# Kernel optimization log

Measured on AMD Instinct MI355X. Metric: run time of the kernel, lower is better.

The kernel has to match this reference:

```python
import jax, jax.numpy as jnp
from jax import lax
import numpy as np

SEQ = 1024
VOCAB = 50000
EMB = 300
CAS_V, CAS_D = 8, 50
POS_V, POS_D = 48, 50
IN_DIM = EMB + CAS_D + POS_D  # 400
H = 512
T = 13  # num_classes / CRF tags


def setup_inputs() -> dict:
    key = jax.random.key(0)
    ks = jax.random.split(key, 16)
    s = lambda k, shape, sc=0.05: jax.random.normal(k, shape, dtype=jnp.float32) * sc
    return {
        "x": jax.random.randint(ks[0], (SEQ,), 0, VOCAB),
        "casing": jax.random.randint(ks[1], (SEQ,), 0, CAS_V),
        "pos": jax.random.randint(ks[2], (SEQ,), 0, POS_V),
        "h0": jnp.zeros((2, H), dtype=jnp.float32),
        "c0": jnp.zeros((2, H), dtype=jnp.float32),
        "W_emb": s(ks[3], (VOCAB, EMB)),
        "W_cas": s(ks[4], (CAS_V, CAS_D)),
        "W_pos": s(ks[5], (POS_V, POS_D)),
        "Wx_f": s(ks[6], (IN_DIM, 4 * H)),
        "Wh_f": s(ks[7], (H, 4 * H)),
        "b_f": jnp.zeros((4 * H,), dtype=jnp.float32),
        "Wx_b": s(ks[8], (IN_DIM, 4 * H)),
        "Wh_b": s(ks[9], (H, 4 * H)),
        "b_b": jnp.zeros((4 * H,), dtype=jnp.float32),
        "W_out": s(ks[10], (2 * H, T)),
        "b_out": jnp.zeros((T,), dtype=jnp.float32),
        "trans": s(ks[11], (T, T), 0.1),
        "start_trans": s(ks[12], (T,), 0.1),
        "end_trans": s(ks[13], (T,), 0.1),
    }


def _lstm_dir(feat, Wx, Wh, b, h0, c0, reverse):
    # feat: [L, IN_DIM]; precompute input projection for all steps
    pre = feat @ Wx + b  # [L, 4H]

    def step(carry, p):
        h, c = carry
        z = p + h @ Wh
        i, f, g, o = jnp.split(z, 4, axis=-1)
        c = jax.nn.sigmoid(f) * c + jax.nn.sigmoid(i) * jnp.tanh(g)
        h = jax.nn.sigmoid(o) * jnp.tanh(c)
        return (h, c), h

    _, hs = lax.scan(step, (h0, c0), pre, reverse=reverse)
    return hs  # [L, H]


def _viterbi(em, trans, start_trans, end_trans):
    # em: [L, T] emission (log) scores; max-plus DP
    score0 = start_trans + em[0]

    def fwd(score, e):
        total = score[:, None] + trans  # [T, T]: prev -> next
        best = jnp.max(total, axis=0) + e
        idx = jnp.argmax(total, axis=0)
        return best, idx

    final, hist = lax.scan(fwd, score0, em[1:])  # hist: [L-1, T]
    final = final + end_trans
    last = jnp.argmax(final)

    def back(tag, idx_row):
        return idx_row[tag], tag

    first, rest = lax.scan(back, last, hist, reverse=True)
    return jnp.concatenate([first[None], rest])  # [L] int


def reference(x, casing, pos, h0, c0, W_emb, W_cas, W_pos, Wx_f, Wh_f, b_f,
              Wx_b, Wh_b, b_b, W_out, b_out, trans, start_trans, end_trans):
    # AWD-LSTM encode (eval mode: dropout identity)
    feat = jnp.concatenate([W_emb[x], W_cas[casing], W_pos[pos]], axis=-1)  # [L, 400]
    hf = _lstm_dir(feat, Wx_f, Wh_f, b_f, h0[0], c0[0], reverse=False)
    hb = _lstm_dir(feat, Wx_b, Wh_b, b_b, h0[1], c0[1], reverse=True)
    o = jnp.concatenate([hf, hb], axis=-1) @ W_out + b_out  # [L, T]
    tag_scores = jax.nn.log_softmax(o, axis=1)
    path = _viterbi(tag_scores, trans, start_trans, end_trans)
    return tag_scores, path
```

## Files before the change

kernel.cpp:

```cpp
#include <hip/hip_runtime.h>
#include <hip/hip_bf16.h>
#include <math.h>

#define SEQ 1024
#define HID 512
#define FOURH 2048
#define IND 400
#define NT 13

#define NWG_DIR 32
#define LSTM_THREADS 512
#define JPW 16
#define WCOLS 64
#define TAG_INVALID 0xFFFFFFFFu

__device__ __forceinline__ float bf2f(unsigned short u) {
    union { unsigned u32; float f; } v;
    v.u32 = ((unsigned)u) << 16;
    return v.f;
}

__device__ __forceinline__ unsigned short f2bf(float f) {
    union { float f; unsigned u; } v;
    v.f = f;
    unsigned u = v.u;
    unsigned rounding = 0x7FFFu + ((u >> 16) & 1u);
    u += rounding;
    return (unsigned short)(u >> 16);
}

__device__ __forceinline__ float ldf(const void* p, size_t i, int isf32) {
    return isf32 ? ((const float*)p)[i] : bf2f(((const unsigned short*)p)[i]);
}

__device__ __forceinline__ float fsigm(float x) {
    return __builtin_amdgcn_rcpf(1.f + __builtin_amdgcn_exp2f(-1.44269504f * x));
}
__device__ __forceinline__ float ftanhf(float x) {
    return 1.f - 2.f * __builtin_amdgcn_rcpf(__builtin_amdgcn_exp2f(2.88539008f * x) + 1.f);
}
__device__ __forceinline__ float satz(float z) { return fminf(fmaxf(z, -60.f), 60.f); }

__global__ __launch_bounds__(64) void detect_kernel(const unsigned short* __restrict__ w,
                                                    int* __restrict__ flag,
                                                    unsigned* __restrict__ vcnt) {
    int lane = threadIdx.x;
    int cnt = 0;
    for (int i = 0; i < 4; ++i) {
        unsigned short u = w[2 * (lane * 4 + i)];
        int e = (u >> 7) & 0xFF;
        if (e >= 90 && e < 127) cnt++;
    }
#pragma unroll
    for (int off = 32; off >= 1; off >>= 1) cnt += __shfl_xor(cnt, off, 64);
    if (lane == 0) *flag = (cnt < 128) ? 1 : 0;
    if (lane == 1) *vcnt = 0;
}

__global__ __launch_bounds__(256) void pre_gemm_kernel(
        const int* __restrict__ x, const int* __restrict__ cas, const int* __restrict__ pos,
        const void* __restrict__ W_emb, const void* __restrict__ W_cas, const void* __restrict__ W_pos,
        const void* __restrict__ Wx_f, const void* __restrict__ b_f,
        const void* __restrict__ Wx_b, const void* __restrict__ b_b,
        unsigned short* __restrict__ pre, const int* __restrict__ dflag) {
    __shared__ float ftile[32 * IND];
    __shared__ int idxs[96];
    const int isf32 = *dflag;
    int dir = blockIdx.z;
    const void* Wx = dir ? Wx_b : Wx_f;
    const void* bb = dir ? b_b : b_f;
    unsigned short* pre_d = pre + (size_t)dir * SEQ * FOURH;
    int r0 = blockIdx.y * 32;
    int col = blockIdx.x * 256 + threadIdx.x;
    int tid = threadIdx.x;

    if (tid < 32)       idxs[tid] = x[r0 + tid];
    else if (tid < 64)  idxs[tid] = cas[r0 + tid - 32];
    else if (tid < 96)  idxs[tid] = pos[r0 + tid - 64];
    __syncthreads();

    for (int idx = tid; idx < 32 * IND; idx += 256) {
        int r = idx / IND;
        int e = idx - r * IND;
        float v;
        if (e < 300)      v = ldf(W_emb, (size_t)idxs[r] * 300 + e, isf32);
        else if (e < 350) v = ldf(W_cas, (size_t)idxs[32 + r] * 50 + (e - 300), isf32);
        else              v = ldf(W_pos, (size_t)idxs[64 + r] * 50 + (e - 350), isf32);
        ftile[idx] = v;
    }
    __syncthreads();

    float acc[32];
    float bias = ldf(bb, col, isf32);
#pragma unroll
    for (int r = 0; r < 32; ++r) acc[r] = bias;

    if (isf32) {
        const float* W = (const float*)Wx;
        for (int kk = 0; kk < 100; ++kk) {
            int k = kk * 4;
            float w0 = W[(size_t)(k + 0) * FOURH + col];
            float w1 = W[(size_t)(k + 1) * FOURH + col];
            float w2 = W[(size_t)(k + 2) * FOURH + col];
            float w3 = W[(size_t)(k + 3) * FOURH + col];
#pragma unroll
            for (int r = 0; r < 32; ++r) {
                float4 f = *(const float4*)&ftile[r * IND + k];
                acc[r] += f.x * w0 + f.y * w1 + f.z * w2 + f.w * w3;
            }
        }
    } else {
        const unsigned short* W = (const unsigned short*)Wx;
        for (int kk = 0; kk < 100; ++kk) {
            int k = kk * 4;
            float w0 = bf2f(W[(size_t)(k + 0) * FOURH + col]);
            float w1 = bf2f(W[(size_t)(k + 1) * FOURH + col]);
            float w2 = bf2f(W[(size_t)(k + 2) * FOURH + col]);
            float w3 = bf2f(W[(size_t)(k + 3) * FOURH + col]);
#pragma unroll
            for (int r = 0; r < 32; ++r) {
                float4 f = *(const float4*)&ftile[r * IND + k];
                acc[r] += f.x * w0 + f.y * w1 + f.z * w2 + f.w * w3;
            }
        }
    }
    for (int r = 0; r < 32; ++r) pre_d[(size_t)(r0 + r) * FOURH + col] = f2bf(acc[r]);
}

__global__ __launch_bounds__(LSTM_THREADS, 2) void lstm_kernel(
        const void* __restrict__ Wh_f, const void* __restrict__ Wh_b,
        const void* __restrict__ h0, const void* __restrict__ c0,
        const unsigned short* __restrict__ pre, float* __restrict__ hsout,
        unsigned long long* hbuf, const int* __restrict__ dflag) {
    __shared__ float red[2][8 * WCOLS];

    const int isf32 = *dflag;
    const int tid = threadIdx.x;
    const int b = blockIdx.x;
    const int dir = b & 1;
    const int g = b >> 1;
    const int j0 = g * JPW;

    const void* Wh = dir ? Wh_b : Wh_f;
    const unsigned short* pre_d = pre + (size_t)dir * SEQ * FOURH;
    float* hso = hsout + (size_t)dir * SEQ * HID;
    unsigned long long* hb_d = hbuf + dir * 2 * HID;

    const int seg  = tid >> 6;
    const int col  = tid & 63;
    const int unit = col & 15;
    const int gate = col >> 4;
    const int gcol = gate * HID + j0 + unit;
    const int redoff = seg * WCOLS + unit * 4 + gate;

    float4 w0, w1, w2, w3, w4, w5, w6, w7, w8, w9, w10, w11, w12, w13, w14, w15;
    if (isf32) {
        const float* wp = (const float*)Wh + (size_t)(seg * 64) * FOURH + gcol;
#define LDW(i) w##i = make_float4(wp[(size_t)(4*i+0)*FOURH], wp[(size_t)(4*i+1)*FOURH], \
                                  wp[(size_t)(4*i+2)*FOURH], wp[(size_t)(4*i+3)*FOURH])
        LDW(0); LDW(1); LDW(2); LDW(3); LDW(4); LDW(5); LDW(6); LDW(7);
        LDW(8); LDW(9); LDW(10); LDW(11); LDW(12); LDW(13); LDW(14); LDW(15);
#undef LDW
    } else {
        const unsigned short* wp = (const unsigned short*)Wh + (size_t)(seg * 64) * FOURH + gcol;
#define LDW(i) w##i = make_float4(bf2f(wp[(size_t)(4*i+0)*FOURH]), bf2f(wp[(size_t)(4*i+1)*FOURH]), \
                                  bf2f(wp[(size_t)(4*i+2)*FOURH]), bf2f(wp[(size_t)(4*i+3)*FOURH]))
        LDW(0); LDW(1); LDW(2); LDW(3); LDW(4); LDW(5); LDW(6); LDW(7);
        LDW(8); LDW(9); LDW(10); LDW(11); LDW(12); LDW(13); LDW(14); LDW(15);
#undef LDW
    }

    float creg = 0.f;
    unsigned short zn0 = 0, zn1 = 0, zn2 = 0, zn3 = 0;
    if (tid < JPW) {
        creg = ldf(c0, dir * HID + j0 + tid, isf32);
        float h0v = ldf(h0, dir * HID + j0 + tid, isf32);
        __hip_atomic_store(&hb_d[j0 + tid],
                           (unsigned long long)__float_as_uint(h0v),
                           __ATOMIC_RELAXED, __HIP_MEMORY_SCOPE_AGENT);
        __hip_atomic_store(&hb_d[HID + j0 + tid],
                           ((unsigned long long)TAG_INVALID << 32),
                           __ATOMIC_RELAXED, __HIP_MEMORY_SCOPE_AGENT);
        int t0 = dir ? (SEQ - 1) : 0;
        zn0 = pre_d[(size_t)t0 * FOURH + 0 * HID + j0 + tid];
        zn1 = pre_d[(size_t)t0 * FOURH + 1 * HID + j0 + tid];
        zn2 = pre_d[(size_t)t0 * FOURH + 2 * HID + j0 + tid];
        zn3 = pre_d[(size_t)t0 * FOURH + 3 * HID + j0 + tid];
    }
    __syncthreads();

    for (int s = 0; s < SEQ; ++s) {
        const int t = dir ? (SEQ - 1 - s) : s;

        unsigned hu;
        {
            const unsigned long long* wp = &hb_d[(s & 1) * HID + tid];
            const unsigned expect = (unsigned)s;
            unsigned long long w;
            do {
                w = __hip_atomic_load(wp, __ATOMIC_RELAXED, __HIP_MEMORY_SCOPE_AGENT);
            } while ((unsigned)(w >> 32) != expect);
            hu = (unsigned)w;
        }

        float zc0 = 0.f, zc1 = 0.f, zc2 = 0.f, zc3 = 0.f;
        if (tid < JPW) {
            zc0 = bf2f(zn0); zc1 = bf2f(zn1); zc2 = bf2f(zn2); zc3 = bf2f(zn3);
            if (s + 1 < SEQ) {
                int tn = dir ? (SEQ - 2 - s) : (s + 1);
                zn0 = pre_d[(size_t)tn * FOURH + 0 * HID + j0 + tid];
                zn1 = pre_d[(size_t)tn * FOURH + 1 * HID + j0 + tid];
                zn2 = pre_d[(size_t)tn * FOURH + 2 * HID + j0 + tid];
                zn3 = pre_d[(size_t)tn * FOURH + 3 * HID + j0 + tid];
            }
        }

        float a0 = 0.f, a1 = 0.f, a2 = 0.f, a3 = 0.f;
#define MACQ(i, A) { \
        float hx = __uint_as_float((unsigned)__builtin_amdgcn_readlane((int)hu, 4*i+0)); \
        float hy = __uint_as_float((unsigned)__builtin_amdgcn_readlane((int)hu, 4*i+1)); \
        float hz = __uint_as_float((unsigned)__builtin_amdgcn_readlane((int)hu, 4*i+2)); \
        float hw = __uint_as_float((unsigned)__builtin_amdgcn_readlane((int)hu, 4*i+3)); \
        A += hx * w##i.x + hy * w##i.y + hz * w##i.z + hw * w##i.w; }
        MACQ(0, a0)  MACQ(1, a1)  MACQ(2, a2)  MACQ(3, a3)
        MACQ(4, a0)  MACQ(5, a1)  MACQ(6, a2)  MACQ(7, a3)
        MACQ(8, a0)  MACQ(9, a1)  MACQ(10, a2) MACQ(11, a3)
        MACQ(12, a0) MACQ(13, a1) MACQ(14, a2) MACQ(15, a3)
#undef MACQ
        red[s & 1][redoff] = (a0 + a1) + (a2 + a3);
        __syncthreads();

        if (tid < JPW) {
            int jj = tid;
            float z0 = zc0, z1 = zc1, z2 = zc2, z3 = zc3;
            const float* rp = &red[s & 1][0];
#pragma unroll
            for (int s8 = 0; s8 < 8; ++s8) {
                float4 r4 = *(const float4*)&rp[s8 * WCOLS + jj * 4];
                z0 += r4.x; z1 += r4.y; z2 += r4.z; z3 += r4.w;
            }
            z0 = satz(z0); z1 = satz(z1); z2 = satz(z2); z3 = satz(z3);
            float ig = fsigm(z0);
            float fg = fsigm(z1);
            float gg = ftanhf(z2);
            float og = fsigm(z3);
            float cnew = fg * creg + ig * gg;
            creg = cnew;
            float hnew = og * ftanhf(satz(cnew));
            unsigned long long w = ((unsigned long long)(unsigned)(s + 1) << 32)
                                 | (unsigned long long)__float_as_uint(hnew);
            __hip_atomic_store(&hb_d[((s + 1) & 1) * HID + j0 + jj], w,
                               __ATOMIC_RELAXED, __HIP_MEMORY_SCOPE_AGENT);
            hso[(size_t)t * HID + j0 + jj] = hnew;
        }
    }
}

__global__ __launch_bounds__(64) void outproj_kernel(const float* __restrict__ hsout,
        const void* __restrict__ W_out, const void* __restrict__ b_out,
        float* __restrict__ out_scores,
        const void* __restrict__ trans, const void* __restrict__ strans,
        const void* __restrict__ etrans, float* __restrict__ out_path,
        unsigned* __restrict__ vcnt, const int* __restrict__ dflag) {
    __shared__ unsigned char hist[SEQ][NT];
    const int isf32 = *dflag;
    int t = blockIdx.x;
    int lane = threadIdx.x;
    const float* hf = hsout + (size_t)t * HID;
    const float* hb = hsout + (size_t)SEQ * HID + (size_t)t * HID;
    float acc[NT];
#pragma unroll
    for (int j = 0; j < NT; ++j) acc[j] = 0.f;
    for (int k = lane; k < HID; k += 64) {
        float a = hf[k], b2 = hb[k];
#pragma unroll
        for (int j = 0; j < NT; ++j)
            acc[j] += a * ldf(W_out, (size_t)k * NT + j, isf32)
                    + b2 * ldf(W_out, (size_t)(HID + k) * NT + j, isf32);
    }
#pragma unroll
    for (int off = 32; off >= 1; off >>= 1) {
#pragma unroll
        for (int j = 0; j < NT; ++j) acc[j] += __shfl_xor(acc[j], off, 64);
    }
    float o[NT];
    float m = -1e30f;
#pragma unroll
    for (int j = 0; j < NT; ++j) { o[j] = acc[j] + ldf(b_out, j, isf32); m = fmaxf(m, o[j]); }
    float lse = 0.f;
#pragma unroll
    for (int j = 0; j < NT; ++j) lse += expf(o[j] - m);
    lse = m + logf(lse);
    if (lane < NT)
        __hip_atomic_store(&out_scores[t * NT + lane], o[lane] - lse,
                           __ATOMIC_RELAXED, __HIP_MEMORY_SCOPE_AGENT);
    __builtin_amdgcn_s_waitcnt(0);

    unsigned old = 0;
    if (lane == 0) old = atomicAdd(vcnt, 1u);
    old = __shfl(old, 0, 64);
    if (old != SEQ - 1) return;

    const float* em = out_scores;
    int j = lane < NT ? lane : 0;
    float tr[NT];
#pragma unroll
    for (int i = 0; i < NT; ++i) tr[i] = ldf(trans, i * NT + j, isf32);
#define EML(tt) __hip_atomic_load(&em[(size_t)(tt) * NT + j], __ATOMIC_RELAXED, __HIP_MEMORY_SCOPE_AGENT)
    float score = ldf(strans, j, isf32) + EML(0);
    float c0 = EML(1), c1 = EML(2), c2 = EML(3), c3 = EML(4),
          c4 = EML(5), c5 = EML(6), c6 = EML(7), c7 = EML(8);
#define VSTEP(PE, TT) { \
    float best = -1e30f; int arg = 0; \
    _Pragma("unroll") \
    for (int i = 0; i < NT; ++i) { \
        float si = __shfl(score, i, 64); \
        float cand = si + tr[i]; \
        if (cand > best) { best = cand; arg = i; } \
    } \
    if (lane < NT) hist[TT][lane] = (unsigned char)arg; \
    score = best + PE; }
    for (int tb = 1; tb < SEQ; tb += 8) {
        int nb = tb + 8;
        float n0 = 0.f, n1 = 0.f, n2 = 0.f, n3 = 0.f, n4 = 0.f, n5 = 0.f, n6 = 0.f, n7 = 0.f;
        if (nb + 0 < SEQ) n0 = EML(nb + 0);
        if (nb + 1 < SEQ) n1 = EML(nb + 1);
        if (nb + 2 < SEQ) n2 = EML(nb + 2);
        if (nb + 3 < SEQ) n3 = EML(nb + 3);
        if (nb + 4 < SEQ) n4 = EML(nb + 4);
        if (nb + 5 < SEQ) n5 = EML(nb + 5);
        if (nb + 6 < SEQ) n6 = EML(nb + 6);
        if (nb + 7 < SEQ) n7 = EML(nb + 7);
        VSTEP(c0, tb + 0)
        if (tb + 1 < SEQ) VSTEP(c1, tb + 1)
        if (tb + 2 < SEQ) VSTEP(c2, tb + 2)
        if (tb + 3 < SEQ) VSTEP(c3, tb + 3)
        if (tb + 4 < SEQ) VSTEP(c4, tb + 4)
        if (tb + 5 < SEQ) VSTEP(c5, tb + 5)
        if (tb + 6 < SEQ) VSTEP(c6, tb + 6)
        if (tb + 7 < SEQ) VSTEP(c7, tb + 7)
        c0 = n0; c1 = n1; c2 = n2; c3 = n3; c4 = n4; c5 = n5; c6 = n6; c7 = n7;
    }
#undef VSTEP
#undef EML
    score += ldf(etrans, j, isf32);
    float bmax = -1e30f;
    int last = 0;
#pragma unroll
    for (int i = 0; i < NT; ++i) {
        float si = __shfl(score, i, 64);
        if (si > bmax) { bmax = si; last = i; }
    }
    if (lane == 0) {
        int cur = last;
        out_path[SEQ - 1] = (float)cur;
        for (int tt = SEQ - 1; tt >= 1; --tt) {
            cur = hist[tt][cur];
            out_path[tt - 1] = (float)cur;
        }
    }
}

extern "C" void kernel_launch(void* const* d_in, const int* in_sizes, int n_in,
                              void* d_out, int out_size, void* d_ws, size_t ws_size,
                              hipStream_t stream) {
    const int* x      = (const int*)d_in[0];
    const int* casing = (const int*)d_in[1];
    const int* posi   = (const int*)d_in[2];
    const void* h0    = d_in[3];
    const void* c0    = d_in[4];
    const void* W_emb = d_in[5];
    const void* W_cas = d_in[6];
    const void* W_pos = d_in[7];
    const void* Wx_f  = d_in[8];
    const void* Wh_f  = d_in[9];
    const void* b_f   = d_in[10];
    const void* Wx_b  = d_in[11];
    const void* Wh_b  = d_in[12];
    const void* b_b   = d_in[13];
    const void* W_out = d_in[14];
    const void* b_out = d_in[15];
    const void* trans = d_in[16];
    const void* strans = d_in[17];
    const void* etrans = d_in[18];

    char* ws = (char*)d_ws;
    int* dflag          = (int*)(ws + 448);
    unsigned* vcnt      = (unsigned*)(ws + 456);
    unsigned short* pre = (unsigned short*)(ws + 512);
    float* hsout        = (float*)(ws + 512 + 8388608);
    unsigned long long* hbuf = (unsigned long long*)(ws + 512 + 8388608 + 4194304);

    float* out_scores = (float*)d_out;
    float* out_path   = out_scores + SEQ * NT;

    detect_kernel<<<1, 64, 0, stream>>>((const unsigned short*)W_emb, dflag, vcnt);

    dim3 g2(8, 32, 2);
    pre_gemm_kernel<<<g2, 256, 0, stream>>>(x, casing, posi, W_emb, W_cas, W_pos,
                                            Wx_f, b_f, Wx_b, b_b, pre, dflag);

    lstm_kernel<<<2 * NWG_DIR, LSTM_THREADS, 0, stream>>>(
        Wh_f, Wh_b, h0, c0, pre, hsout, hbuf, dflag);

    outproj_kernel<<<SEQ, 64, 0, stream>>>(hsout, W_out, b_out, out_scores,
                                           trans, strans, etrans, out_path, vcnt, dflag);
}
```

Measured before the change: 2.334 ms.

## Replicate LSTM hidden-state exchange buffer per consumer workgroup to spread polling

The recurrent hidden-state handoff buffer is replicated once per workgroup in each direction. Each producer thread writes its new h value (tagged with the step number) into all 32 replicas, and each workgroup spin-polls only its own private copy. The goal is to stop all workgroups of a direction from polling the same cache lines, which should cut coherence traffic and latency in the per-step cross-workgroup sync. The first step now reads h0 directly instead of waiting on the buffer. The cost is 32 times more atomic stores per producer per step, and a much larger hbuf that the host allocation must supply.

```diff
diff --git a/kernel.cpp b/kernel.cpp
--- a/kernel.cpp
+++ b/kernel.cpp
@@ -144,7 +144,8 @@
     const void* Wh = dir ? Wh_b : Wh_f;
     const unsigned short* pre_d = pre + (size_t)dir * SEQ * FOURH;
     float* hso = hsout + (size_t)dir * SEQ * HID;
-    unsigned long long* hb_d = hbuf + dir * 2 * HID;
+    unsigned long long* hb_dir = hbuf + (size_t)dir * NWG_DIR * 2 * HID;
+    unsigned long long* hb_my  = hb_dir + (size_t)g * 2 * HID;
 
     const int seg  = tid >> 6;
     const int col  = tid & 63;
@@ -170,17 +171,19 @@
 #undef LDW
     }
 
+    const unsigned hu0 = __float_as_uint(ldf(h0, dir * HID + tid, isf32));
+
     float creg = 0.f;
     unsigned short zn0 = 0, zn1 = 0, zn2 = 0, zn3 = 0;
     if (tid < JPW) {
         creg = ldf(c0, dir * HID + j0 + tid, isf32);
-        float h0v = ldf(h0, dir * HID + j0 + tid, isf32);
-        __hip_atomic_store(&hb_d[j0 + tid],
-                           (unsigned long long)__float_as_uint(h0v),
-                           __ATOMIC_RELAXED, __HIP_MEMORY_SCOPE_AGENT);
-        __hip_atomic_store(&hb_d[HID + j0 + tid],
-                           ((unsigned long long)TAG_INVALID << 32),
-                           __ATOMIC_RELAXED, __HIP_MEMORY_SCOPE_AGENT);
+        const unsigned long long iv = ((unsigned long long)TAG_INVALID << 32);
+#pragma unroll
+        for (int c = 0; c < NWG_DIR; ++c) {
+            unsigned long long* base = hb_dir + (size_t)c * 2 * HID + j0 + tid;
+            __hip_atomic_store(base,       iv, __ATOMIC_RELAXED, __HIP_MEMORY_SCOPE_AGENT);
+            __hip_atomic_store(base + HID, iv, __ATOMIC_RELAXED, __HIP_MEMORY_SCOPE_AGENT);
+        }
         int t0 = dir ? (SEQ - 1) : 0;
         zn0 = pre_d[(size_t)t0 * FOURH + 0 * HID + j0 + tid];
         zn1 = pre_d[(size_t)t0 * FOURH + 1 * HID + j0 + tid];
@@ -193,8 +196,10 @@
         const int t = dir ? (SEQ - 1 - s) : s;
 
         unsigned hu;
-        {
-            const unsigned long long* wp = &hb_d[(s & 1) * HID + tid];
+        if (s == 0) {
+            hu = hu0;
+        } else {
+            const unsigned long long* wp = &hb_my[(s & 1) * HID + tid];
             const unsigned expect = (unsigned)s;
             unsigned long long w;
             do {
@@ -249,8 +254,12 @@
             float hnew = og * ftanhf(satz(cnew));
             unsigned long long w = ((unsigned long long)(unsigned)(s + 1) << 32)
                                  | (unsigned long long)__float_as_uint(hnew);
-            __hip_atomic_store(&hb_d[((s + 1) & 1) * HID + j0 + jj], w,
-                               __ATOMIC_RELAXED, __HIP_MEMORY_SCOPE_AGENT);
+            const int par = (s + 1) & 1;
+            unsigned long long* dst = hb_dir + (size_t)par * HID + j0 + jj;
+#pragma unroll
+            for (int c = 0; c < NWG_DIR; ++c)
+                __hip_atomic_store(dst + (size_t)c * 2 * HID, w,
+                                   __ATOMIC_RELAXED, __HIP_MEMORY_SCOPE_AGENT);
             hso[(size_t)t * HID + j0 + jj] = hnew;
         }
     }
```

New measurement: 2.859 ms. +22.5%, slower.

## Split LSTM recurrence into 512 single-wave blocks with shuffle reduction

Applied to the files above, without the earlier changes.

Restructures the persistent LSTM kernel from 64 workgroups of 512 threads into 512 single-wavefront workgroups, each owning two hidden units per direction. Each lane polls eight h entries and reduces with cross-lane shuffles, so the shared-memory reduction and the __syncthreads barrier go away. In exchange, every wave polls all 512 h values itself, and each step needs all 512 workgroups co-resident and synchronising through global memory. Together these multiply the polling traffic across the device.

```diff
diff --git a/kernel.cpp b/kernel.cpp
--- a/kernel.cpp
+++ b/kernel.cpp
@@ -8,10 +8,6 @@
 #define IND 400
 #define NT 13
 
-#define NWG_DIR 32
-#define LSTM_THREADS 512
-#define JPW 16
-#define WCOLS 64
 #define TAG_INVALID 0xFFFFFFFFu
 
 __device__ __forceinline__ float bf2f(unsigned short u) {
@@ -127,118 +123,116 @@
     for (int r = 0; r < 32; ++r) pre_d[(size_t)(r0 + r) * FOURH + col] = f2bf(acc[r]);
 }
 
-__global__ __launch_bounds__(LSTM_THREADS, 2) void lstm_kernel(
+__global__ __launch_bounds__(64) void lstm_kernel(
         const void* __restrict__ Wh_f, const void* __restrict__ Wh_b,
         const void* __restrict__ h0, const void* __restrict__ c0,
         const unsigned short* __restrict__ pre, float* __restrict__ hsout,
         unsigned long long* hbuf, const int* __restrict__ dflag) {
-    __shared__ float red[2][8 * WCOLS];
-
     const int isf32 = *dflag;
-    const int tid = threadIdx.x;
+    const int lane = threadIdx.x;
     const int b = blockIdx.x;
     const int dir = b & 1;
-    const int g = b >> 1;
-    const int j0 = g * JPW;
+    const int wid = b >> 1;
+    const int u0 = wid * 2;
 
     const void* Wh = dir ? Wh_b : Wh_f;
     const unsigned short* pre_d = pre + (size_t)dir * SEQ * FOURH;
     float* hso = hsout + (size_t)dir * SEQ * HID;
     unsigned long long* hb_d = hbuf + dir * 2 * HID;
 
-    const int seg  = tid >> 6;
-    const int col  = tid & 63;
-    const int unit = col & 15;
-    const int gate = col >> 4;
-    const int gcol = gate * HID + j0 + unit;
-    const int redoff = seg * WCOLS + unit * 4 + gate;
-
-    float4 w0, w1, w2, w3, w4, w5, w6, w7, w8, w9, w10, w11, w12, w13, w14, w15;
+    float4 w0a, w1a, w2a, w3a, w4a, w5a, w6a, w7a;
+    float4 w0b, w1b, w2b, w3b, w4b, w5b, w6b, w7b;
     if (isf32) {
-        const float* wp = (const float*)Wh + (size_t)(seg * 64) * FOURH + gcol;
-#define LDW(i) w##i = make_float4(wp[(size_t)(4*i+0)*FOURH], wp[(size_t)(4*i+1)*FOURH], \
-                                  wp[(size_t)(4*i+2)*FOURH], wp[(size_t)(4*i+3)*FOURH])
-        LDW(0); LDW(1); LDW(2); LDW(3); LDW(4); LDW(5); LDW(6); LDW(7);
-        LDW(8); LDW(9); LDW(10); LDW(11); LDW(12); LDW(13); LDW(14); LDW(15);
-#undef LDW
+        const float* W = (const float*)Wh;
+#define LDWI(i) { const float* p = W + (size_t)(lane + 64 * i) * FOURH; \
+        w##i##a = make_float4(p[0 * HID + u0], p[0 * HID + u0 + 1], p[1 * HID + u0], p[1 * HID + u0 + 1]); \
+        w##i##b = make_float4(p[2 * HID + u0], p[2 * HID + u0 + 1], p[3 * HID + u0], p[3 * HID + u0 + 1]); }
+        LDWI(0) LDWI(1) LDWI(2) LDWI(3) LDWI(4) LDWI(5) LDWI(6) LDWI(7)
+#undef LDWI
     } else {
-        const unsigned short* wp = (const unsigned short*)Wh + (size_t)(seg * 64) * FOURH + gcol;
-#define LDW(i) w##i = make_float4(bf2f(wp[(size_t)(4*i+0)*FOURH]), bf2f(wp[(size_t)(4*i+1)*FOURH]), \
-                                  bf2f(wp[(size_t)(4*i+2)*FOURH]), bf2f(wp[(size_t)(4*i+3)*FOURH]))
-        LDW(0); LDW(1); LDW(2); LDW(3); LDW(4); LDW(5); LDW(6); LDW(7);
-        LDW(8); LDW(9); LDW(10); LDW(11); LDW(12); LDW(13); LDW(14); LDW(15);
-#undef LDW
+        const unsigned short* W = (const unsigned short*)Wh;
+#define LDWI(i) { const unsigned short* p = W + (size_t)(lane + 64 * i) * FOURH; \
+        w##i##a = make_float4(bf2f(p[0 * HID + u0]), bf2f(p[0 * HID + u0 + 1]), bf2f(p[1 * HID + u0]), bf2f(p[1 * HID + u0 + 1])); \
+        w##i##b = make_float4(bf2f(p[2 * HID + u0]), bf2f(p[2 * HID + u0 + 1]), bf2f(p[3 * HID + u0]), bf2f(p[3 * HID + u0 + 1])); }
+        LDWI(0) LDWI(1) LDWI(2) LDWI(3) LDWI(4) LDWI(5) LDWI(6) LDWI(7)
+#undef LDWI
     }
 
     float creg = 0.f;
     unsigned short zn0 = 0, zn1 = 0, zn2 = 0, zn3 = 0;
-    if (tid < JPW) {
-        creg = ldf(c0, dir * HID + j0 + tid, isf32);
-        float h0v = ldf(h0, dir * HID + j0 + tid, isf32);
-        __hip_atomic_store(&hb_d[j0 + tid],
+    if (lane < 2) {
+        creg = ldf(c0, dir * HID + u0 + lane, isf32);
+        float h0v = ldf(h0, dir * HID + u0 + lane, isf32);
+        __hip_atomic_store(&hb_d[u0 + lane],
                            (unsigned long long)__float_as_uint(h0v),
                            __ATOMIC_RELAXED, __HIP_MEMORY_SCOPE_AGENT);
-        __hip_atomic_store(&hb_d[HID + j0 + tid],
+        __hip_atomic_store(&hb_d[HID + u0 + lane],
                            ((unsigned long long)TAG_INVALID << 32),
                            __ATOMIC_RELAXED, __HIP_MEMORY_SCOPE_AGENT);
         int t0 = dir ? (SEQ - 1) : 0;
-        zn0 = pre_d[(size_t)t0 * FOURH + 0 * HID + j0 + tid];
-        zn1 = pre_d[(size_t)t0 * FOURH + 1 * HID + j0 + tid];
-        zn2 = pre_d[(size_t)t0 * FOURH + 2 * HID + j0 + tid];
-        zn3 = pre_d[(size_t)t0 * FOURH + 3 * HID + j0 + tid];
-    }
-    __syncthreads();
+        zn0 = pre_d[(size_t)t0 * FOURH + 0 * HID + u0 + lane];
+        zn1 = pre_d[(size_t)t0 * FOURH + 1 * HID + u0 + lane];
+        zn2 = pre_d[(size_t)t0 * FOURH + 2 * HID + u0 + lane];
+        zn3 = pre_d[(size_t)t0 * FOURH + 3 * HID + u0 + lane];
+    }
+    asm volatile("s_waitcnt vmcnt(0)" ::: "memory");
 
     for (int s = 0; s < SEQ; ++s) {
         const int t = dir ? (SEQ - 1 - s) : s;
 
-        unsigned hu;
-        {
-            const unsigned long long* wp = &hb_d[(s & 1) * HID + tid];
-            const unsigned expect = (unsigned)s;
-            unsigned long long w;
-            do {
-                w = __hip_atomic_load(wp, __ATOMIC_RELAXED, __HIP_MEMORY_SCOPE_AGENT);
-            } while ((unsigned)(w >> 32) != expect);
-            hu = (unsigned)w;
-        }
+        const unsigned long long* base = &hb_d[(s & 1) * HID + lane];
+        const unsigned e = (unsigned)s;
+#define LDP(off) __hip_atomic_load(base + (off), __ATOMIC_RELAXED, __HIP_MEMORY_SCOPE_AGENT)
+        unsigned long long v0 = LDP(0),   v1 = LDP(64),  v2 = LDP(128), v3 = LDP(192),
+                           v4 = LDP(256), v5 = LDP(320), v6 = LDP(384), v7 = LDP(448);
+        while (!((unsigned)(v0 >> 32) == e && (unsigned)(v1 >> 32) == e &&
+                 (unsigned)(v2 >> 32) == e && (unsigned)(v3 >> 32) == e &&
+                 (unsigned)(v4 >> 32) == e && (unsigned)(v5 >> 32) == e &&
+                 (unsigned)(v6 >> 32) == e && (unsigned)(v7 >> 32) == e)) {
+            if ((unsigned)(v0 >> 32) != e) v0 = LDP(0);
+            if ((unsigned)(v1 >> 32) != e) v1 = LDP(64);
+            if ((unsigned)(v2 >> 32) != e) v2 = LDP(128);
+            if ((unsigned)(v3 >> 32) != e) v3 = LDP(192);
+            if ((unsigned)(v4 >> 32) != e) v4 = LDP(256);
+            if ((unsigned)(v5 >> 32) != e) v5 = LDP(320);
+            if ((unsigned)(v6 >> 32) != e) v6 = LDP(384);
+            if ((unsigned)(v7 >> 32) != e) v7 = LDP(448);
+        }
+#undef LDP
 
         float zc0 = 0.f, zc1 = 0.f, zc2 = 0.f, zc3 = 0.f;
-        if (tid < JPW) {
+        if (lane < 2) {
             zc0 = bf2f(zn0); zc1 = bf2f(zn1); zc2 = bf2f(zn2); zc3 = bf2f(zn3);
             if (s + 1 < SEQ) {
                 int tn = dir ? (SEQ - 2 - s) : (s + 1);
-                zn0 = pre_d[(size_t)tn * FOURH + 0 * HID + j0 + tid];
-                zn1 = pre_d[(size_t)tn * FOURH + 1 * HID + j0 + tid];
-                zn2 = pre_d[(size_t)tn * FOURH + 2 * HID + j0 + tid];
-                zn3 = pre_d[(size_t)tn * FOURH + 3 * HID + j0 + tid];
+                zn0 = pre_d[(size_t)tn * FOURH + 0 * HID + u0 + lane];
+                zn1 = pre_d[(size_t)tn * FOURH + 1 * HID + u0 + lane];
+                zn2 = pre_d[(size_t)tn * FOURH + 2 * HID + u0 + lane];
+                zn3 = pre_d[(size_t)tn * FOURH + 3 * HID + u0 + lane];
             }
         }
 
-        float a0 = 0.f, a1 = 0.f, a2 = 0.f, a3 = 0.f;
-#define MACQ(i, A) { \
-        float hx = __uint_as_float((unsigned)__builtin_amdgcn_readlane((int)hu, 4*i+0)); \
-        float hy = __uint_as_float((unsigned)__builtin_amdgcn_readlane((int)hu, 4*i+1)); \
-        float hz = __uint_as_float((unsigned)__builtin_amdgcn_readlane((int)hu, 4*i+2)); \
-        float hw = __uint_as_float((unsigned)__builtin_amdgcn_readlane((int)hu, 4*i+3)); \
-        A += hx * w##i.x + hy * w##i.y + hz * w##i.z + hw * w##i.w; }
-        MACQ(0, a0)  MACQ(1, a1)  MACQ(2, a2)  MACQ(3, a3)
-        MACQ(4, a0)  MACQ(5, a1)  MACQ(6, a2)  MACQ(7, a3)
-        MACQ(8, a0)  MACQ(9, a1)  MACQ(10, a2) MACQ(11, a3)
-        MACQ(12, a0) MACQ(13, a1) MACQ(14, a2) MACQ(15, a3)
-#undef MACQ
-        red[s & 1][redoff] = (a0 + a1) + (a2 + a3);
-        __syncthreads();
-
-        if (tid < JPW) {
-            int jj = tid;
-            float z0 = zc0, z1 = zc1, z2 = zc2, z3 = zc3;
-            const float* rp = &red[s & 1][0];
-#pragma unroll
-            for (int s8 = 0; s8 < 8; ++s8) {
-                float4 r4 = *(const float4*)&rp[s8 * WCOLS + jj * 4];
-                z0 += r4.x; z1 += r4.y; z2 += r4.z; z3 += r4.w;
-            }
+        float aAx = 0.f, aAy = 0.f, aAz = 0.f, aAw = 0.f;
+        float aBx = 0.f, aBy = 0.f, aBz = 0.f, aBw = 0.f;
+#define MACI(i) { float hf = __uint_as_float((unsigned)v##i); \
+        aAx += hf * w##i##a.x; aAy += hf * w##i##a.y; aAz += hf * w##i##a.z; aAw += hf * w##i##a.w; \
+        aBx += hf * w##i##b.x; aBy += hf * w##i##b.y; aBz += hf * w##i##b.z; aBw += hf * w##i##b.w; }
+        MACI(0) MACI(1) MACI(2) MACI(3) MACI(4) MACI(5) MACI(6) MACI(7)
+#undef MACI
+
+#define RED(off) { \
+        aAx += __shfl_xor(aAx, off, 64); aAy += __shfl_xor(aAy, off, 64); \
+        aAz += __shfl_xor(aAz, off, 64); aAw += __shfl_xor(aAw, off, 64); \
+        aBx += __shfl_xor(aBx, off, 64); aBy += __shfl_xor(aBy, off, 64); \
+        aBz += __shfl_xor(aBz, off, 64); aBw += __shfl_xor(aBw, off, 64); }
+        RED(1) RED(2) RED(4) RED(8) RED(16) RED(32)
+#undef RED
+
+        if (lane < 2) {
+            float z0 = (lane ? aAy : aAx) + zc0;
+            float z1 = (lane ? aAw : aAz) + zc1;
+            float z2 = (lane ? aBy : aBx) + zc2;
+            float z3 = (lane ? aBw : aBz) + zc3;
             z0 = satz(z0); z1 = satz(z1); z2 = satz(z2); z3 = satz(z3);
             float ig = fsigm(z0);
             float fg = fsigm(z1);
@@ -249,9 +243,9 @@
             float hnew = og * ftanhf(satz(cnew));
             unsigned long long w = ((unsigned long long)(unsigned)(s + 1) << 32)
                                  | (unsigned long long)__float_as_uint(hnew);
-            __hip_atomic_store(&hb_d[((s + 1) & 1) * HID + j0 + jj], w,
+            __hip_atomic_store(&hb_d[((s + 1) & 1) * HID + u0 + lane], w,
                                __ATOMIC_RELAXED, __HIP_MEMORY_SCOPE_AGENT);
-            hso[(size_t)t * HID + j0 + jj] = hnew;
+            hso[(size_t)t * HID + u0 + lane] = hnew;
         }
     }
 }
@@ -400,7 +394,7 @@
     pre_gemm_kernel<<<g2, 256, 0, stream>>>(x, casing, posi, W_emb, W_cas, W_pos,
                                             Wx_f, b_f, Wx_b, b_b, pre, dflag);
 
-    lstm_kernel<<<2 * NWG_DIR, LSTM_THREADS, 0, stream>>>(
+    lstm_kernel<<<512, 64, 0, stream>>>(
         Wh_f, Wh_b, h0, c0, pre, hsout, hbuf, dflag);
 
     outproj_kernel<<<SEQ, 64, 0, stream>>>(hsout, W_out, b_out, out_scores,
```

Measured after the change: 4.589 ms. 1.97x slower.

## Spread LSTM gate epilogue over 64 lanes and duplicate hidden-state exchange buffers

Applied to the files above, without the earlier changes.

The per-step epilogue now uses 64 lanes, one per (unit, gate), instead of 16 lanes each doing four gates. Each lane sums its own column of the reduction and applies its activation, and the four gate values are gathered with xor shuffles. The hidden-state publish is written to two copies of the exchange buffer, and consumers poll both, alternating. This is meant to shorten the serial critical path of each recurrent step and cut polling latency, at the cost of extra atomic stores and loads. It also relies on the hbuf allocation being large enough for a second copy at offset 4096.

```diff
diff --git a/kernel.cpp b/kernel.cpp
--- a/kernel.cpp
+++ b/kernel.cpp
@@ -144,7 +144,8 @@
     const void* Wh = dir ? Wh_b : Wh_f;
     const unsigned short* pre_d = pre + (size_t)dir * SEQ * FOURH;
     float* hso = hsout + (size_t)dir * SEQ * HID;
-    unsigned long long* hb_d = hbuf + dir * 2 * HID;
+    unsigned long long* hb_d  = hbuf + dir * 2 * HID;
+    unsigned long long* hb2_d = hbuf + 4096 + dir * 2 * HID;
 
     const int seg  = tid >> 6;
     const int col  = tid & 63;
@@ -152,6 +153,11 @@
     const int gate = col >> 4;
     const int gcol = gate * HID + j0 + unit;
     const int redoff = seg * WCOLS + unit * 4 + gate;
+
+    const int isep  = (tid < 64);
+    const int eunit = tid >> 2;
+    const int egate = tid & 3;
+    const int ispub = isep && (egate == 0);
 
     float4 w0, w1, w2, w3, w4, w5, w6, w7, w8, w9, w10, w11, w12, w13, w14, w15;
     if (isf32) {
@@ -171,21 +177,20 @@
     }
 
     float creg = 0.f;
-    unsigned short zn0 = 0, zn1 = 0, zn2 = 0, zn3 = 0;
-    if (tid < JPW) {
-        creg = ldf(c0, dir * HID + j0 + tid, isf32);
-        float h0v = ldf(h0, dir * HID + j0 + tid, isf32);
-        __hip_atomic_store(&hb_d[j0 + tid],
-                           (unsigned long long)__float_as_uint(h0v),
-                           __ATOMIC_RELAXED, __HIP_MEMORY_SCOPE_AGENT);
-        __hip_atomic_store(&hb_d[HID + j0 + tid],
-                           ((unsigned long long)TAG_INVALID << 32),
-                           __ATOMIC_RELAXED, __HIP_MEMORY_SCOPE_AGENT);
+    unsigned short zn = 0;
+    if (isep) {
+        if (ispub) {
+            creg = ldf(c0, dir * HID + j0 + eunit, isf32);
+            float h0v = ldf(h0, dir * HID + j0 + eunit, isf32);
+            unsigned long long wv = (unsigned long long)__float_as_uint(h0v);
+            unsigned long long iv = ((unsigned long long)TAG_INVALID << 32);
+            __hip_atomic_store(&hb_d[j0 + eunit],        wv, __ATOMIC_RELAXED, __HIP_MEMORY_SCOPE_AGENT);
+            __hip_atomic_store(&hb2_d[j0 + eunit],       wv, __ATOMIC_RELAXED, __HIP_MEMORY_SCOPE_AGENT);
+            __hip_atomic_store(&hb_d[HID + j0 + eunit],  iv, __ATOMIC_RELAXED, __HIP_MEMORY_SCOPE_AGENT);
+            __hip_atomic_store(&hb2_d[HID + j0 + eunit], iv, __ATOMIC_RELAXED, __HIP_MEMORY_SCOPE_AGENT);
+        }
         int t0 = dir ? (SEQ - 1) : 0;
-        zn0 = pre_d[(size_t)t0 * FOURH + 0 * HID + j0 + tid];
-        zn1 = pre_d[(size_t)t0 * FOURH + 1 * HID + j0 + tid];
-        zn2 = pre_d[(size_t)t0 * FOURH + 2 * HID + j0 + tid];
-        zn3 = pre_d[(size_t)t0 * FOURH + 3 * HID + j0 + tid];
+        zn = pre_d[(size_t)t0 * FOURH + egate * HID + j0 + eunit];
     }
     __syncthreads();
 
@@ -194,24 +199,25 @@
 
         unsigned hu;
         {
-            const unsigned long long* wp = &hb_d[(s & 1) * HID + tid];
+            const unsigned long long* A = &hb_d[(s & 1) * HID + tid];
+            const unsigned long long* B = &hb2_d[(s & 1) * HID + tid];
             const unsigned expect = (unsigned)s;
-            unsigned long long w;
-            do {
-                w = __hip_atomic_load(wp, __ATOMIC_RELAXED, __HIP_MEMORY_SCOPE_AGENT);
-            } while ((unsigned)(w >> 32) != expect);
-            hu = (unsigned)w;
-        }
-
-        float zc0 = 0.f, zc1 = 0.f, zc2 = 0.f, zc3 = 0.f;
-        if (tid < JPW) {
-            zc0 = bf2f(zn0); zc1 = bf2f(zn1); zc2 = bf2f(zn2); zc3 = bf2f(zn3);
+            unsigned long long va = __hip_atomic_load(A, __ATOMIC_RELAXED, __HIP_MEMORY_SCOPE_AGENT);
+            unsigned long long vb = __hip_atomic_load(B, __ATOMIC_RELAXED, __HIP_MEMORY_SCOPE_AGENT);
+            for (;;) {
+                if ((unsigned)(va >> 32) == expect) { hu = (unsigned)va; break; }
+                va = __hip_atomic_load(A, __ATOMIC_RELAXED, __HIP_MEMORY_SCOPE_AGENT);
+                if ((unsigned)(vb >> 32) == expect) { hu = (unsigned)vb; break; }
+                vb = __hip_atomic_load(B, __ATOMIC_RELAXED, __HIP_MEMORY_SCOPE_AGENT);
+            }
+        }
+
+        float zc = 0.f;
+        if (isep) {
+            zc = bf2f(zn);
             if (s + 1 < SEQ) {
                 int tn = dir ? (SEQ - 2 - s) : (s + 1);
-                zn0 = pre_d[(size_t)tn * FOURH + 0 * HID + j0 + tid];
-                zn1 = pre_d[(size_t)tn * FOURH + 1 * HID + j0 + tid];
-                zn2 = pre_d[(size_t)tn * FOURH + 2 * HID + j0 + tid];
-                zn3 = pre_d[(size_t)tn * FOURH + 3 * HID + j0 + tid];
+                zn = pre_d[(size_t)tn * FOURH + egate * HID + j0 + eunit];
             }
         }
 
@@ -230,28 +236,33 @@
         red[s & 1][redoff] = (a0 + a1) + (a2 + a3);
         __syncthreads();
 
-        if (tid < JPW) {
-            int jj = tid;
-            float z0 = zc0, z1 = zc1, z2 = zc2, z3 = zc3;
+        if (isep) {
             const float* rp = &red[s & 1][0];
-#pragma unroll
-            for (int s8 = 0; s8 < 8; ++s8) {
-                float4 r4 = *(const float4*)&rp[s8 * WCOLS + jj * 4];
-                z0 += r4.x; z1 += r4.y; z2 += r4.z; z3 += r4.w;
+            float z = rp[0 * WCOLS + tid] + rp[1 * WCOLS + tid]
+                    + rp[2 * WCOLS + tid] + rp[3 * WCOLS + tid]
+                    + rp[4 * WCOLS + tid] + rp[5 * WCOLS + tid]
+                    + rp[6 * WCOLS + tid] + rp[7 * WCOLS + tid];
+            z = satz(z + zc);
+            float vs = fsigm(z);
+            float vt = ftanhf(z);
+            float v = (egate == 2) ? vt : vs;
+            float x1 = __shfl_xor(v, 1, 64);
+            float x2 = __shfl_xor(v, 2, 64);
+            float x3 = __shfl_xor(x1, 2, 64);
+            if (ispub) {
+                float ig = v, fg = x1, gg = x2, og = x3;
+                float cnew = fg * creg + ig * gg;
+                creg = cnew;
+                float hnew = og * ftanhf(satz(cnew));
+                unsigned long long w = ((unsigned long long)(unsigned)(s + 1) << 32)
+                                     | (unsigned long long)__float_as_uint(hnew);
+                const int par = (s + 1) & 1;
+                __hip_atomic_store(&hb_d[par * HID + j0 + eunit], w,
+                                   __ATOMIC_RELAXED, __HIP_MEMORY_SCOPE_AGENT);
+                __hip_atomic_store(&hb2_d[par * HID + j0 + eunit], w,
+                                   __ATOMIC_RELAXED, __HIP_MEMORY_SCOPE_AGENT);
+                hso[(size_t)t * HID + j0 + eunit] = hnew;
             }
-            z0 = satz(z0); z1 = satz(z1); z2 = satz(z2); z3 = satz(z3);
-            float ig = fsigm(z0);
-            float fg = fsigm(z1);
-            float gg = ftanhf(z2);
-            float og = fsigm(z3);
-            float cnew = fg * creg + ig * gg;
-            creg = cnew;
-            float hnew = og * ftanhf(satz(cnew));
-            unsigned long long w = ((unsigned long long)(unsigned)(s + 1) << 32)
-                                 | (unsigned long long)__float_as_uint(hnew);
-            __hip_atomic_store(&hb_d[((s + 1) & 1) * HID + j0 + jj], w,
-                               __ATOMIC_RELAXED, __HIP_MEMORY_SCOPE_AGENT);
-            hso[(size_t)t * HID + j0 + jj] = hnew;
         }
     }
 }
```

Result: faster. 2.281 ms (-2.3%).
